# Kernel optimization log

Hardware: AMD Instinct MI355X
Metric: run time of the kernel (lower is better)

## Reference

```python
import jax, jax.numpy as jnp
import numpy as np

HEADS = 16

def setup_inputs() -> dict:
    key = jax.random.key(0)
    k1, k2, k3 = jax.random.split(key, 3)
    T, B, E = 2048, 4, 1024
    query = jax.random.normal(k1, (T, B, E), dtype=jnp.float32)
    in_proj_weight = jax.random.normal(k2, (3 * E, E), dtype=jnp.float32) * (E ** -0.5)
    out_proj_weight = jax.random.normal(k3, (E, E), dtype=jnp.float32) * (E ** -0.5)
    return {"query": query, "in_proj_weight": in_proj_weight, "out_proj_weight": out_proj_weight}

def reference(query, in_proj_weight, out_proj_weight):
    # query: [T, B, E] (time-first, as in apex SelfMultiheadAttn)
    T, B, E = query.shape
    H = HEADS
    D = E // H
    scale = D ** -0.5
    # fused in-projection: x @ W_in^T -> [T, B, 3E]
    qkv = jnp.einsum('tbe,fe->tbf', query, in_proj_weight)
    q, k, v = jnp.split(qkv, 3, axis=-1)
    # [T, B, E] -> [B, H, T, D]
    def to_bhtd(x):
        return x.reshape(T, B, H, D).transpose(1, 2, 0, 3)
    q = to_bhtd(q) * scale
    k = to_bhtd(k)
    v = to_bhtd(v)
    scores = jnp.einsum('bhqd,bhkd->bhqk', q, k)  # [B, H, T, T]
    # causal (mask_future_timesteps=True) time mask
    causal = jnp.tril(jnp.ones((T, T), dtype=bool))
    scores = jnp.where(causal, scores, jnp.finfo(scores.dtype).min)
    attn = jax.nn.softmax(scores, axis=-1)
    # dropout_prob = 0.0 -> identity
    ctx = jnp.einsum('bhqk,bhkd->bhqd', attn, v)  # [B, H, T, D]
    ctx = ctx.transpose(2, 0, 1, 3).reshape(T, B, E)
    out = jnp.einsum('tbe,fe->tbf', ctx, out_proj_weight)
    return out
```

## Files before the change

kernel.cpp:

```cpp
#include <hip/hip_runtime.h>


typedef float  f32x4  __attribute__((ext_vector_type(4)));
typedef short  s16x8  __attribute__((ext_vector_type(8)));
typedef __bf16 bf16x8 __attribute__((ext_vector_type(8)));

#define T_DIM 2048
#define B_DIM 4
#define E_DIM 1024
#define PLANE (T_DIM * 64)

__device__ inline unsigned short f2bf(float f) {
  return (unsigned short)((__builtin_bit_cast(unsigned int, f) + 0x8000u) >> 16);
}

__device__ inline f32x4 mfma16(s16x8 a, s16x8 b, f32x4 c) {
  return __builtin_amdgcn_mfma_f32_16x16x32_bf16(
      __builtin_bit_cast(bf16x8, a), __builtin_bit_cast(bf16x8, b), c, 0, 0, 0);
}

__device__ inline void gl2lds16(const unsigned short* g, unsigned short* l) {
  __builtin_amdgcn_global_load_lds(
      (__attribute__((address_space(1))) unsigned int*)g,
      (__attribute__((address_space(3))) unsigned int*)l, 16, 0, 0);
}

__device__ inline unsigned packbf(float a, float b) {
  return __builtin_amdgcn_perm(__builtin_bit_cast(unsigned, b),
                               __builtin_bit_cast(unsigned, a), 0x07060302u);
}

__global__ __launch_bounds__(256)
void cvt_bf16(const float* __restrict__ in, unsigned short* __restrict__ out,
              int n4) {
  int i = blockIdx.x * 256 + threadIdx.x;
  if (i >= n4) return;
  float4 v = ((const float4*)in)[i];
  ushort4 o;
  o.x = f2bf(v.x); o.y = f2bf(v.y); o.z = f2bf(v.z); o.w = f2bf(v.w);
  ((ushort4*)out)[i] = o;
}

__global__ __launch_bounds__(256)
void cvt_w_in(const float* __restrict__ in, unsigned short* __restrict__ out,
              float qs) {
  int i = blockIdx.x * 256 + threadIdx.x;
  float sc = (i < (E_DIM * E_DIM / 4)) ? qs : 1.0f;
  float4 v = ((const float4*)in)[i];
  ushort4 o;
  o.x = f2bf(v.x * sc); o.y = f2bf(v.y * sc);
  o.z = f2bf(v.z * sc); o.w = f2bf(v.w * sc);
  ((ushort4*)out)[i] = o;
}

__global__ __launch_bounds__(256, 2)
void gemm256(const unsigned short* __restrict__ A,
             const unsigned short* __restrict__ Bw,
             unsigned short* __restrict__ Cq, int K) {
  __shared__ __attribute__((aligned(16))) unsigned short As[256 * 64];
  __shared__ __attribute__((aligned(16))) unsigned short Bs[128 * 64];

  const int tid = threadIdx.x, lane = tid & 63, w = tid >> 6;
  const int row16 = lane & 15, quad = lane >> 4;
  const int m0 = blockIdx.y * 256, n0 = blockIdx.x * 128;
  const int wm = (w & 1) * 128, wn = (w >> 1) * 64;
  const int srow = lane >> 3;
  const int jsw = (lane & 7) ^ srow;
  const int sw7 = row16 & 7;

  f32x4 acc[8][4];
  for (int i = 0; i < 8; ++i)
    for (int j = 0; j < 4; ++j) acc[i][j] = (f32x4){0.f, 0.f, 0.f, 0.f};

  for (int k0 = 0; k0 < K; k0 += 64) {
    for (int i2 = 0; i2 < 8; ++i2) {
      int ia = w * 8 + i2;
      int r = ia * 8 + srow;
      gl2lds16(A + (size_t)(m0 + r) * K + k0 + jsw * 8, &As[ia * 512]);
    }
    for (int i2 = 0; i2 < 4; ++i2) {
      int ib = w * 4 + i2;
      int r = ib * 8 + srow;
      gl2lds16(Bw + (size_t)(n0 + r) * K + k0 + jsw * 8, &Bs[ib * 512]);
    }
    __syncthreads();
    for (int kk = 0; kk < 2; ++kk) {
      s16x8 af[8], bfr[4];
      for (int mi = 0; mi < 8; ++mi)
        af[mi] = *(const s16x8*)&As[(wm + mi * 16 + row16) * 64 +
                                    (((kk * 4 + quad) ^ sw7) * 8)];
      for (int ni = 0; ni < 4; ++ni)
        bfr[ni] = *(const s16x8*)&Bs[(wn + ni * 16 + row16) * 64 +
                                     (((kk * 4 + quad) ^ sw7) * 8)];
      for (int mi = 0; mi < 8; ++mi)
        for (int ni = 0; ni < 4; ++ni)
          acc[mi][ni] = mfma16(af[mi], bfr[ni], acc[mi][ni]);
    }
    __syncthreads();
  }

  if (n0 >= 2048) {
    const int hw = ((n0 & 1023) >> 6) + (w >> 1);
    const int tg0 = (m0 >> 2) + (w & 1) * 32;
    unsigned short* tb = &As[w * 2560];
    for (int bb = 0; bb < 4; ++bb) {
      for (int mi = 0; mi < 8; ++mi)
        for (int ni = 0; ni < 4; ++ni)
          tb[(ni * 16 + row16) * 40 + mi * 4 + quad] = f2bf(acc[mi][ni][bb]);
      asm volatile("s_waitcnt lgkmcnt(0)" ::: "memory");
      unsigned short* vp = Cq + (size_t)(128 + bb * 16 + hw) * PLANE;
      for (int it = 0; it < 4; ++it) {
        int dd = it * 16 + (lane >> 2);
        int tl = (lane & 3) * 8;
        s16x8 v = *(const s16x8*)&tb[dd * 40 + tl];
        *(s16x8*)(vp + (size_t)dd * T_DIM + tg0 + tl) = v;
      }
      asm volatile("s_waitcnt lgkmcnt(0)" ::: "memory");
    }
  } else {
    for (int mi = 0; mi < 8; ++mi)
      for (int ni = 0; ni < 4; ++ni)
        for (int r = 0; r < 4; ++r) {
          int m = m0 + wm + mi * 16 + quad * 4 + r;
          int n = n0 + wn + ni * 16 + row16;
          int t = m >> 2, bb = m & 3;
          int which = n >> 10, hh = (n >> 6) & 15, dd = n & 63;
          Cq[(size_t)(which * 64 + bb * 16 + hh) * PLANE + (size_t)t * 64 + dd] =
              f2bf(acc[mi][ni][r]);
        }
  }
}

__global__ __launch_bounds__(256)
void gemm128(const unsigned short* __restrict__ A,
             const unsigned short* __restrict__ Bw,
             float* __restrict__ Cf, int N, int K) {
  __shared__ __attribute__((aligned(16))) unsigned short As[128 * 64];
  __shared__ __attribute__((aligned(16))) unsigned short Bs[128 * 64];

  const int tid = threadIdx.x, lane = tid & 63, w = tid >> 6;
  const int row16 = lane & 15, quad = lane >> 4;
  const int m0 = blockIdx.y * 128, n0 = blockIdx.x * 128;
  const int wm = (w & 1) * 64, wn = (w >> 1) * 64;
  const int srow = lane >> 3;
  const int jsw = (lane & 7) ^ srow;
  const int sw7 = row16 & 7;

  f32x4 acc[4][4];
  for (int i = 0; i < 4; ++i)
    for (int j = 0; j < 4; ++j) acc[i][j] = (f32x4){0.f, 0.f, 0.f, 0.f};

  for (int k0 = 0; k0 < K; k0 += 64) {
    for (int i = 0; i < 4; ++i) {
      int ia = i * 4 + w;
      int r = ia * 8 + srow;
      gl2lds16(A  + (size_t)(m0 + r) * K + k0 + jsw * 8, &As[ia * 512]);
      gl2lds16(Bw + (size_t)(n0 + r) * K + k0 + jsw * 8, &Bs[ia * 512]);
    }
    __syncthreads();
    for (int kk = 0; kk < 2; ++kk) {
      s16x8 af[4], bfr[4];
      for (int mi = 0; mi < 4; ++mi)
        af[mi] = *(const s16x8*)&As[(wm + mi * 16 + row16) * 64 +
                                    (((kk * 4 + quad) ^ sw7) * 8)];
      for (int ni = 0; ni < 4; ++ni)
        bfr[ni] = *(const s16x8*)&Bs[(wn + ni * 16 + row16) * 64 +
                                     (((kk * 4 + quad) ^ sw7) * 8)];
      for (int mi = 0; mi < 4; ++mi)
        for (int ni = 0; ni < 4; ++ni)
          acc[mi][ni] = mfma16(af[mi], bfr[ni], acc[mi][ni]);
    }
    __syncthreads();
  }

  for (int mi = 0; mi < 4; ++mi)
    for (int ni = 0; ni < 4; ++ni)
      for (int r = 0; r < 4; ++r) {
        int m = m0 + wm + mi * 16 + quad * 4 + r;
        int n = n0 + wn + ni * 16 + row16;
        Cf[(size_t)m * N + n] = acc[mi][ni][r];
      }
}

__global__ __launch_bounds__(256)
void attn_fwd(const unsigned short* __restrict__ qkv,
              unsigned short* __restrict__ ctx) {
  __shared__ __attribute__((aligned(16))) unsigned short Ks[4][4096];
  __shared__ __attribute__((aligned(16))) unsigned short Vs[4][4096];
  __shared__ __attribute__((aligned(16))) unsigned short Ps[4][2048];

  const int tid = threadIdx.x, lane = tid & 63, w = tid >> 6;
  const int row16 = lane & 15, quad = lane >> 4;
  const int bh = blockIdx.x;
  const int p  = blockIdx.y;
  const int b = bh >> 4, h = bh & 15;

  const unsigned short* Qg = qkv + (size_t)bh * PLANE;
  const unsigned short* Kg = qkv + (size_t)(64 + bh) * PLANE;
  const unsigned short* Vt = qkv + (size_t)(128 + bh) * PLANE;

  const int r8 = lane >> 3;
  const int jsw = (lane & 7) ^ r8;
  const int sw7 = row16 & 7;

  auto stage = [&](int c, int buf) {
    for (int i2 = 0; i2 < 2; ++i2) {
      int i = w + i2 * 4;
      int r = i * 8 + r8;
      gl2lds16(Kg + (size_t)(c * 64 + r) * 64 + jsw * 8, &Ks[buf][i * 512]);
      gl2lds16(Vt + (size_t)r * T_DIM + c * 64 + jsw * 8, &Vs[buf][i * 512]);
    }
  };

  for (int half = 0; half < 2; ++half) {
    const int qt = half ? p : (15 - p);
    const int q0w = qt * 128 + w * 32;
    const int cmax = 2 * qt + 1;
    const int dc = 2 * qt + (w >> 1);

    s16x8 qb[2][2];
    for (int nq = 0; nq < 2; ++nq)
      for (int s = 0; s < 2; ++s)
        qb[nq][s] = *(const s16x8*)(Qg + (size_t)(q0w + nq * 16 + row16) * 64 +
                                    s * 32 + quad * 8);

    f32x4 O[4][2];
    for (int md = 0; md < 4; ++md)
      for (int nq = 0; nq < 2; ++nq) O[md][nq] = (f32x4){0.f, 0.f, 0.f, 0.f};
    float lp[2] = {0.f, 0.f};

    if (half) __builtin_amdgcn_s_barrier();
    stage(0, 0);
    stage(1, 1);
    if (cmax >= 2) stage(2, 2);

    for (int c = 0; c <= cmax; ++c) {
      const int buf = c & 3;
      const int rem = cmax - c;
      if (rem >= 2)      asm volatile("s_waitcnt vmcnt(8)" ::: "memory");
      else if (rem == 1) asm volatile("s_waitcnt vmcnt(4)" ::: "memory");
      else               asm volatile("s_waitcnt vmcnt(0)" ::: "memory");
      __builtin_amdgcn_s_barrier();
      if (c + 3 <= cmax) stage(c + 3, (c + 3) & 3);

      if (c <= dc) {
        f32x4 S[4][2];
        for (int nt = 0; nt < 4; ++nt)
          for (int nq = 0; nq < 2; ++nq) S[nt][nq] = (f32x4){0.f, 0.f, 0.f, 0.f};
        __builtin_amdgcn_s_setprio(1);
        for (int nt = 0; nt < 4; ++nt)
          for (int s = 0; s < 2; ++s) {
            s16x8 ka = *(const s16x8*)&Ks[buf][(nt * 16 + row16) * 64 +
                                              (((s * 4 + quad) ^ sw7) * 8)];
            for (int nq = 0; nq < 2; ++nq)
              S[nt][nq] = mfma16(ka, qb[nq][s], S[nt][nq]);
          }
        __builtin_amdgcn_s_setprio(0);

        auto softmax_store = [&](bool diagm) {
          for (int nq = 0; nq < 2; ++nq) {
            const int qg = q0w + nq * 16 + row16;
            for (int nt = 0; nt < 4; ++nt) {
              float pv[4];
              for (int r = 0; r < 4; ++r) {
                pv[r] = __builtin_amdgcn_exp2f(S[nt][nq][r]);
                if (diagm && (c * 64 + nt * 16 + quad * 4 + r) > qg) pv[r] = 0.f;
                lp[nq] += pv[r];
              }
              int qr = nq * 16 + row16;
              int pos = (nt * 2 + (quad >> 1)) ^ sw7;
              *(uint2*)&Ps[w][qr * 64 + pos * 8 + (quad & 1) * 4] =
                  make_uint2(packbf(pv[0], pv[1]), packbf(pv[2], pv[3]));
            }
          }
        };
        if (c == dc) softmax_store(true); else softmax_store(false);
        asm volatile("s_waitcnt lgkmcnt(0)" ::: "memory");

        __builtin_amdgcn_s_setprio(1);
        for (int sk = 0; sk < 2; ++sk) {
          s16x8 pb[2];
          for (int nq = 0; nq < 2; ++nq)
            pb[nq] = *(const s16x8*)&Ps[w][(nq * 16 + row16) * 64 +
                                           (((sk * 4 + quad) ^ sw7) * 8)];
          for (int md = 0; md < 4; ++md) {
            s16x8 va = *(const s16x8*)&Vs[buf][(md * 16 + row16) * 64 +
                                              (((sk * 4 + quad) ^ sw7) * 8)];
            for (int nq = 0; nq < 2; ++nq)
              O[md][nq] = mfma16(va, pb[nq], O[md][nq]);
          }
        }
        __builtin_amdgcn_s_setprio(0);
      }
    }

    for (int nq = 0; nq < 2; ++nq) {
      float s = lp[nq];
      s += __shfl_xor(s, 16);
      s += __shfl_xor(s, 32);
      float inv = 1.f / s;
      const int t = q0w + nq * 16 + row16;
      for (int md = 0; md < 4; ++md) {
        unsigned lo = packbf(O[md][nq][0] * inv, O[md][nq][1] * inv);
        unsigned hi = packbf(O[md][nq][2] * inv, O[md][nq][3] * inv);
        *(uint2*)&ctx[((size_t)t * B_DIM + b) * E_DIM + h * 64 + md * 16 +
                      quad * 4] = make_uint2(lo, hi);
      }
    }
  }
}

extern "C" void kernel_launch(void* const* d_in, const int* in_sizes, int n_in,
                              void* d_out, int out_size, void* d_ws,
                              size_t ws_size, hipStream_t stream) {
  const float* query = (const float*)d_in[0];
  const float* win   = (const float*)d_in[1];
  const float* wout  = (const float*)d_in[2];
  float* out = (float*)d_out;

  unsigned short* qkvb = (unsigned short*)d_ws;
  unsigned short* ctxb = qkvb + (size_t)3 * B_DIM * 16 * T_DIM * 64;
  unsigned short* xb   = ctxb;
  unsigned short* winb = (unsigned short*)d_out;
  unsigned short* woutb = qkvb;

  const float QSCALE = 0.18033688011112042f;

  cvt_bf16<<<8192, 256, 0, stream>>>(query, xb, (8192 * 1024) / 4);
  cvt_w_in<<<3072, 256, 0, stream>>>(win, winb, QSCALE);
  gemm256<<<dim3(3072 / 128, 8192 / 256), 256, 0, stream>>>(xb, winb, qkvb,
                                                            1024);
  attn_fwd<<<dim3(64, 8), 256, 0, stream>>>(qkvb, ctxb);
  cvt_bf16<<<1024, 256, 0, stream>>>(wout, woutb, (1024 * 1024) / 4);
  gemm128<<<dim3(8, 64), 256, 0, stream>>>(ctxb, woutb, out, 1024, 1024);
}
```

Measured before the change: 243.8 us.

## Fuse input conversions into one launch and shrink attention K/V staging to double buffer

Merges the query, in-projection weight and (when the workspace is large enough) out-projection weight fp32-to-bf16 conversions into one kernel launch, removing separate launches. The attention kernel cuts K/V LDS staging from four buffers to two, prefetching chunk c+2 after an extra barrier at the end of each iteration. This lowers LDS use, which may raise occupancy, but shortens the prefetch distance and adds a barrier per chunk.

New measurement: 232.5 us. 1.05x faster.

```diff
diff --git a/kernel.cpp b/kernel.cpp
--- a/kernel.cpp
+++ b/kernel.cpp
@@ -28,6 +28,32 @@
 __device__ inline unsigned packbf(float a, float b) {
   return __builtin_amdgcn_perm(__builtin_bit_cast(unsigned, b),
                                __builtin_bit_cast(unsigned, a), 0x07060302u);
+}
+
+__global__ __launch_bounds__(256)
+void cvt_all(const float* __restrict__ q, const float* __restrict__ wi,
+             const float* __restrict__ wo, unsigned short* __restrict__ xb,
+             unsigned short* __restrict__ wib, unsigned short* __restrict__ wob,
+             float qs, int do_wout) {
+  int blk = blockIdx.x;
+  const float* src;
+  unsigned short* dst;
+  int i;
+  float sc = 1.0f;
+  if (blk < 8192) {
+    src = q; dst = xb; i = blk * 256 + threadIdx.x;
+  } else if (blk < 11264) {
+    src = wi; dst = wib; i = (blk - 8192) * 256 + threadIdx.x;
+    if (i < (E_DIM * E_DIM / 4)) sc = qs;
+  } else {
+    if (!do_wout) return;
+    src = wo; dst = wob; i = (blk - 11264) * 256 + threadIdx.x;
+  }
+  float4 v = ((const float4*)src)[i];
+  ushort4 o;
+  o.x = f2bf(v.x * sc); o.y = f2bf(v.y * sc);
+  o.z = f2bf(v.z * sc); o.w = f2bf(v.w * sc);
+  ((ushort4*)dst)[i] = o;
 }
 
 __global__ __launch_bounds__(256)
@@ -38,18 +64,6 @@
   float4 v = ((const float4*)in)[i];
   ushort4 o;
   o.x = f2bf(v.x); o.y = f2bf(v.y); o.z = f2bf(v.z); o.w = f2bf(v.w);
-  ((ushort4*)out)[i] = o;
-}
-
-__global__ __launch_bounds__(256)
-void cvt_w_in(const float* __restrict__ in, unsigned short* __restrict__ out,
-              float qs) {
-  int i = blockIdx.x * 256 + threadIdx.x;
-  float sc = (i < (E_DIM * E_DIM / 4)) ? qs : 1.0f;
-  float4 v = ((const float4*)in)[i];
-  ushort4 o;
-  o.x = f2bf(v.x * sc); o.y = f2bf(v.y * sc);
-  o.z = f2bf(v.z * sc); o.w = f2bf(v.w * sc);
   ((ushort4*)out)[i] = o;
 }
 
@@ -185,8 +199,8 @@
 __global__ __launch_bounds__(256)
 void attn_fwd(const unsigned short* __restrict__ qkv,
               unsigned short* __restrict__ ctx) {
-  __shared__ __attribute__((aligned(16))) unsigned short Ks[4][4096];
-  __shared__ __attribute__((aligned(16))) unsigned short Vs[4][4096];
+  __shared__ __attribute__((aligned(16))) unsigned short Ks[2][4096];
+  __shared__ __attribute__((aligned(16))) unsigned short Vs[2][4096];
   __shared__ __attribute__((aligned(16))) unsigned short Ps[4][2048];
 
   const int tid = threadIdx.x, lane = tid & 63, w = tid >> 6;
@@ -229,19 +243,14 @@
       for (int nq = 0; nq < 2; ++nq) O[md][nq] = (f32x4){0.f, 0.f, 0.f, 0.f};
     float lp[2] = {0.f, 0.f};
 
-    if (half) __builtin_amdgcn_s_barrier();
     stage(0, 0);
     stage(1, 1);
-    if (cmax >= 2) stage(2, 2);
 
     for (int c = 0; c <= cmax; ++c) {
-      const int buf = c & 3;
-      const int rem = cmax - c;
-      if (rem >= 2)      asm volatile("s_waitcnt vmcnt(8)" ::: "memory");
-      else if (rem == 1) asm volatile("s_waitcnt vmcnt(4)" ::: "memory");
-      else               asm volatile("s_waitcnt vmcnt(0)" ::: "memory");
+      const int buf = c & 1;
+      if (c < cmax) asm volatile("s_waitcnt vmcnt(4)" ::: "memory");
+      else          asm volatile("s_waitcnt vmcnt(0)" ::: "memory");
       __builtin_amdgcn_s_barrier();
-      if (c + 3 <= cmax) stage(c + 3, (c + 3) & 3);
 
       if (c <= dc) {
         f32x4 S[4][2];
@@ -292,6 +301,9 @@
         }
         __builtin_amdgcn_s_setprio(0);
       }
+
+      __builtin_amdgcn_s_barrier();
+      if (c + 2 <= cmax) stage(c + 2, buf);
     }
 
     for (int nq = 0; nq < 2; ++nq) {
@@ -318,19 +330,25 @@
   const float* wout  = (const float*)d_in[2];
   float* out = (float*)d_out;
 
+  const size_t qkv_el = (size_t)3 * 64 * PLANE;
+  const size_t ctx_el = (size_t)T_DIM * B_DIM * E_DIM;
+
   unsigned short* qkvb = (unsigned short*)d_ws;
-  unsigned short* ctxb = qkvb + (size_t)3 * B_DIM * 16 * T_DIM * 64;
+  unsigned short* ctxb = qkvb + qkv_el;
   unsigned short* xb   = ctxb;
   unsigned short* winb = (unsigned short*)d_out;
-  unsigned short* woutb = qkvb;
+
+  const bool big_ws = ws_size >= (qkv_el + ctx_el + (size_t)E_DIM * E_DIM) * 2;
+  unsigned short* woutb = big_ws ? (ctxb + ctx_el) : qkvb;
 
   const float QSCALE = 0.18033688011112042f;
 
-  cvt_bf16<<<8192, 256, 0, stream>>>(query, xb, (8192 * 1024) / 4);
-  cvt_w_in<<<3072, 256, 0, stream>>>(win, winb, QSCALE);
+  cvt_all<<<big_ws ? 12288 : 11264, 256, 0, stream>>>(
+      query, win, wout, xb, winb, woutb, QSCALE, big_ws ? 1 : 0);
   gemm256<<<dim3(3072 / 128, 8192 / 256), 256, 0, stream>>>(xb, winb, qkvb,
                                                             1024);
   attn_fwd<<<dim3(64, 8), 256, 0, stream>>>(qkvb, ctxb);
-  cvt_bf16<<<1024, 256, 0, stream>>>(wout, woutb, (1024 * 1024) / 4);
+  if (!big_ws)
+    cvt_bf16<<<1024, 256, 0, stream>>>(wout, woutb, (1024 * 1024) / 4);
   gemm128<<<dim3(8, 64), 256, 0, stream>>>(ctxb, woutb, out, 1024, 1024);
 }
```
